# Optimization experiments

Hardware: AMD Instinct MI355X
Metric: run time of the kernel (lower is better)

The kernel has to match this reference:

```python
import jax, jax.numpy as jnp
import numpy as np

WS = 8          # window size
NH = 8          # num heads
DIM = 256
HD = DIM // NH  # head dim = 32
SCALE = HD ** -0.5
EPS = 1e-5


def _rel_pos_index(ws):
    # deterministic int index buffer, same math as the torch __init__
    coords = jnp.stack(jnp.meshgrid(jnp.arange(ws), jnp.arange(ws), indexing='ij'))  # [2,ws,ws]
    cf = coords.reshape(2, -1)                     # [2, N]
    rel = cf[:, :, None] - cf[:, None, :]          # [2, N, N]
    return (rel[0] + ws - 1) * (2 * ws - 1) + (rel[1] + ws - 1)  # [N, N]


def _ln(h, g, b):
    m = jnp.mean(h, axis=-1, keepdims=True)
    v = jnp.mean((h - m) ** 2, axis=-1, keepdims=True)
    return (h - m) / jnp.sqrt(v + EPS) * g + b


def setup_inputs() -> dict:
    key = jax.random.key(0)
    ks = jax.random.split(key, 16)
    B_, N, D = 4096, WS * WS, DIM
    s = 0.02
    return {
        'x':      jax.random.normal(ks[0], (B_, N, D), jnp.float32),
        # enhanced qkv: Linear(D,2D) -> LN -> GELU -> Linear(2D,3D)
        'w_qkv1': jax.random.normal(ks[1], (D, 2 * D), jnp.float32) * s,
        'b_qkv1': jnp.zeros((2 * D,), jnp.float32),
        'g_qkv':  jnp.ones((2 * D,), jnp.float32),
        'be_qkv': jnp.zeros((2 * D,), jnp.float32),
        'w_qkv2': jax.random.normal(ks[2], (2 * D, 3 * D), jnp.float32) * s,
        'b_qkv2': jnp.zeros((3 * D,), jnp.float32),
        # relative position bias table [(2*WS-1)^2, NH]
        'rpb':    jax.random.normal(ks[3], ((2 * WS - 1) ** 2, NH), jnp.float32) * s,
        # enhanced proj: Linear(D,2D) -> LN -> GELU -> Linear(2D,D)
        'w_p1':   jax.random.normal(ks[4], (D, 2 * D), jnp.float32) * s,
        'b_p1':   jnp.zeros((2 * D,), jnp.float32),
        'g_p':    jnp.ones((2 * D,), jnp.float32),
        'be_p':   jnp.zeros((2 * D,), jnp.float32),
        'w_p2':   jax.random.normal(ks[5], (2 * D, D), jnp.float32) * s,
        'b_p2':   jnp.zeros((D,), jnp.float32),
    }


def reference(x, w_qkv1, b_qkv1, g_qkv, be_qkv, w_qkv2, b_qkv2, rpb,
              w_p1, b_p1, g_p, be_p, w_p2, b_p2):
    B_, N, C = x.shape
    # enhanced QKV chain: Linear -> LayerNorm -> GELU -> Linear
    h = jax.nn.gelu(_ln(x @ w_qkv1 + b_qkv1, g_qkv, be_qkv), approximate=False)
    qkv = h @ w_qkv2 + b_qkv2                              # [B_, N, 3C]
    qkv = qkv.reshape(B_, N, 3, NH, HD).transpose(2, 0, 3, 1, 4)  # [3, B_, H, N, hd]
    q, k, v = qkv[0], qkv[1], qkv[2]
    attn = jnp.einsum('bhnd,bhmd->bhnm', q * SCALE, k)     # [B_, H, N, N]
    idx = _rel_pos_index(WS)                                # [N, N] int
    bias = rpb[idx.reshape(-1)].reshape(N, N, NH).transpose(2, 0, 1)  # [H, N, N]
    attn = jax.nn.softmax(attn + bias[None], axis=-1)
    out = jnp.einsum('bhnm,bhmd->bhnd', attn, v)           # [B_, H, N, hd]
    out = out.transpose(0, 2, 1, 3).reshape(B_, N, C)
    # enhanced proj chain: Linear -> LayerNorm -> GELU -> Linear
    h = jax.nn.gelu(_ln(out @ w_p1 + b_p1, g_p, be_p), approximate=False)
    return h @ w_p2 + b_p2
```

## Files before the change

### kernel.cpp

```cpp
#include <hip/hip_runtime.h>


typedef __bf16 bf16_t;
typedef __bf16 bf16x8 __attribute__((ext_vector_type(8)));
typedef __bf16 bf16x4 __attribute__((ext_vector_type(4)));
typedef float f32x4 __attribute__((ext_vector_type(4)));

__device__ __forceinline__ f32x4 mfma16(bf16x8 a, bf16x8 b, f32x4 acc) {
  return __builtin_amdgcn_mfma_f32_16x16x32_bf16(a, b, acc, 0, 0, 0);
}

#define SWZ(row, byteoff) ((byteoff) ^ (((row) & 7) << 4))

__device__ __forceinline__ float gelu_f(float v) {
  float e = __expf(v * (1.59576912f + 0.07135482f * v * v));
  return v - v * __builtin_amdgcn_rcpf(1.0f + e);
}

__global__ void wtrans_kernel(const float* __restrict__ src, bf16_t* __restrict__ dst,
                              int kshift, int N, int total) {
  int i = blockIdx.x * 256 + threadIdx.x;
  if (i >= total) return;
  int K = 1 << kshift;
  int k = i & (K - 1);
  int n = i >> kshift;
  dst[i] = (bf16_t)src[(size_t)k * N + n];
}

__global__ void biastab_kernel(const float* __restrict__ rpb, float* __restrict__ bt) {
  int e = blockIdx.x * 256 + threadIdx.x;
  int hd = e >> 12, i = (e >> 6) & 63, j = e & 63;
  int idx = ((i >> 3) - (j >> 3) + 7) * 15 + ((i & 7) - (j & 7) + 7);
  bt[e] = rpb[idx * 8 + hd];
}

__device__ __forceinline__ void gemmT_ln_gelu(
    const char* bsrc, const bf16_t* __restrict__ wt,
    const float* __restrict__ bias, const float* __restrict__ gamma,
    const float* __restrict__ beta,
    char* dst, int flb, float2* part, int wave, int g, int c)
{
  f32x4 acc[4][4] = {};
#pragma unroll
  for (int kt = 0; kt < 8; ++kt) {
    bf16x8 a[4], b[4];
#pragma unroll
    for (int mt = 0; mt < 4; ++mt)
      a[mt] = *(const bf16x8*)(wt + (size_t)(wave * 64 + mt * 16 + c) * 256 + kt * 32 + g * 8);
#pragma unroll
    for (int nt = 0; nt < 4; ++nt) {
      int T = nt * 16 + c;
      b[nt] = *(const bf16x8*)(bsrc + SWZ(T, T * 512 + kt * 64 + g * 16));
    }
#pragma unroll
    for (int mt = 0; mt < 4; ++mt)
#pragma unroll
      for (int nt = 0; nt < 4; ++nt)
        acc[mt][nt] = mfma16(a[mt], b[nt], acc[mt][nt]);
  }
  float s[4] = {0.f, 0.f, 0.f, 0.f}, ss[4] = {0.f, 0.f, 0.f, 0.f};
#pragma unroll
  for (int mt = 0; mt < 4; ++mt) {
    float4 b4 = *(const float4*)(bias + wave * 64 + mt * 16 + g * 4);
#pragma unroll
    for (int nt = 0; nt < 4; ++nt)
#pragma unroll
      for (int r = 0; r < 4; ++r) {
        float v = acc[mt][nt][r] + ((const float*)&b4)[r];
        acc[mt][nt][r] = v;
        s[nt] += v;
        ss[nt] += v * v;
      }
  }
#pragma unroll
  for (int nt = 0; nt < 4; ++nt) {
    float sv = s[nt], ssv = ss[nt];
    sv += __shfl_xor(sv, 16, 64); ssv += __shfl_xor(ssv, 16, 64);
    sv += __shfl_xor(sv, 32, 64); ssv += __shfl_xor(ssv, 32, 64);
    if (g == 0) part[wave * 64 + nt * 16 + c] = make_float2(sv, ssv);
  }
  __syncthreads();
#pragma unroll
  for (int nt = 0; nt < 4; ++nt) {
    float sv = 0.f, ssv = 0.f;
#pragma unroll
    for (int w = 0; w < 8; ++w) {
      float2 p2 = part[w * 64 + nt * 16 + c];
      sv += p2.x; ssv += p2.y;
    }
    float m = sv * (1.f / 512.f);
    float rstd = rsqrtf(ssv * (1.f / 512.f) - m * m + 1e-5f);
#pragma unroll
    for (int mt = 0; mt < 4; ++mt)
#pragma unroll
      for (int r = 0; r < 4; ++r)
        acc[mt][nt][r] = (acc[mt][nt][r] - m) * rstd;
  }
#pragma unroll
  for (int mt = 0; mt < 4; ++mt) {
    float4 g4 = *(const float4*)(gamma + wave * 64 + mt * 16 + g * 4);
    float4 be4 = *(const float4*)(beta + wave * 64 + mt * 16 + g * 4);
    int f0 = flb + mt * 16 + g * 4;
#pragma unroll
    for (int nt = 0; nt < 4; ++nt) {
      int T = nt * 16 + c;
      bf16x4 h4;
#pragma unroll
      for (int r = 0; r < 4; ++r) {
        float v = acc[mt][nt][r] * ((const float*)&g4)[r] + ((const float*)&be4)[r];
        h4[r] = (bf16_t)gelu_f(v);
      }
      *(bf16x4*)(dst + SWZ(T, T * 512 + f0 * 2)) = h4;
    }
  }
}

__global__ __launch_bounds__(512, 2) void g1qa_kernel(
    const float* __restrict__ x,
    const bf16_t* __restrict__ w1t, const float* __restrict__ b1,
    const float* __restrict__ gamma1, const float* __restrict__ beta1,
    const bf16_t* __restrict__ w2t, const float* __restrict__ b2,
    const float* __restrict__ bt,
    bf16_t* __restrict__ ao)
{
  __shared__ __align__(16) char sm[69632];
  char* rA = sm;
  char* rB = sm + 32768;
  float2* part = (float2*)(sm + 65536);
  const int tid = threadIdx.x;
  const int wave = tid >> 6, lane = tid & 63;
  const int g = lane >> 4, c = lane & 15;
  const int win = blockIdx.x;
  const int head = wave;

  const float* xw = x + (size_t)win * 16384;
#pragma unroll
  for (int it = 0; it < 8; ++it) {
    int e = it * 2048 + tid * 4;
    float4 v = *(const float4*)(xw + e);
    int row = e >> 8, col = e & 255;
    bf16x4 t4;
    t4[0] = (bf16_t)v.x; t4[1] = (bf16_t)v.y; t4[2] = (bf16_t)v.z; t4[3] = (bf16_t)v.w;
    *(bf16x4*)(rA + SWZ(row, row * 512 + col * 2)) = t4;
  }
  __syncthreads();
  gemmT_ln_gelu(rA, w1t, b1, gamma1, beta1, (wave < 4) ? rB : rA, (wave & 3) * 64,
                part, wave, g, c);
  __syncthreads();

  bf16x4 vreg[2][4], qreg[2][4], kreg[2][4];

  {
    f32x4 acc[2][4] = {};
#pragma unroll
    for (int kt = 0; kt < 16; ++kt) {
      const char* hb = (kt < 8) ? rB : rA;
      const int ko = (kt & 7) * 64 + g * 16;
      bf16x8 a[2], b[4];
#pragma unroll
      for (int mt = 0; mt < 2; ++mt)
        a[mt] = *(const bf16x8*)(w2t + (size_t)(512 + head * 32 + mt * 16 + c) * 512 + kt * 32 + g * 8);
#pragma unroll
      for (int nt = 0; nt < 4; ++nt) {
        int T = nt * 16 + c;
        b[nt] = *(const bf16x8*)(hb + SWZ(T, T * 512 + ko));
      }
#pragma unroll
      for (int mt = 0; mt < 2; ++mt)
#pragma unroll
        for (int nt = 0; nt < 4; ++nt)
          acc[mt][nt] = mfma16(a[mt], b[nt], acc[mt][nt]);
    }
#pragma unroll
    for (int mt = 0; mt < 2; ++mt) {
      float4 b4 = *(const float4*)(b2 + 512 + head * 32 + mt * 16 + g * 4);
#pragma unroll
      for (int nt = 0; nt < 4; ++nt) {
        bf16x4 o4;
#pragma unroll
        for (int r = 0; r < 4; ++r)
          o4[r] = (bf16_t)(acc[mt][nt][r] + ((const float*)&b4)[r]);
        vreg[mt][nt] = o4;
      }
    }
  }
  {
    f32x4 acc[2][4] = {};
#pragma unroll
    for (int kt = 0; kt < 16; ++kt) {
      const char* hb = (kt < 8) ? rB : rA;
      const int ko = (kt & 7) * 64 + g * 16;
      bf16x8 a[2], b[4];
#pragma unroll
      for (int mt = 0; mt < 2; ++mt)
        a[mt] = *(const bf16x8*)(w2t + (size_t)(head * 32 + mt * 16 + c) * 512 + kt * 32 + g * 8);
#pragma unroll
      for (int nt = 0; nt < 4; ++nt) {
        int T = nt * 16 + c;
        b[nt] = *(const bf16x8*)(hb + SWZ(T, T * 512 + ko));
      }
#pragma unroll
      for (int mt = 0; mt < 2; ++mt)
#pragma unroll
        for (int nt = 0; nt < 4; ++nt)
          acc[mt][nt] = mfma16(a[mt], b[nt], acc[mt][nt]);
    }
#pragma unroll
    for (int mt = 0; mt < 2; ++mt) {
      float4 b4 = *(const float4*)(b2 + head * 32 + mt * 16 + g * 4);
#pragma unroll
      for (int nt = 0; nt < 4; ++nt) {
        bf16x4 o4;
#pragma unroll
        for (int r = 0; r < 4; ++r)
          o4[r] = (bf16_t)((acc[mt][nt][r] + ((const float*)&b4)[r]) * 0.17677669529663687f);
        qreg[mt][nt] = o4;
      }
    }
  }
  {
    f32x4 acc[2][4] = {};
#pragma unroll
    for (int kt = 0; kt < 16; ++kt) {
      const char* hb = (kt < 8) ? rB : rA;
      const int ko = (kt & 7) * 64 + g * 16;
      bf16x8 a[2], b[4];
#pragma unroll
      for (int mt = 0; mt < 2; ++mt)
        a[mt] = *(const bf16x8*)(w2t + (size_t)(256 + head * 32 + mt * 16 + c) * 512 + kt * 32 + g * 8);
#pragma unroll
      for (int nt = 0; nt < 4; ++nt) {
        int T = nt * 16 + c;
        b[nt] = *(const bf16x8*)(hb + SWZ(T, T * 512 + ko));
      }
#pragma unroll
      for (int mt = 0; mt < 2; ++mt)
#pragma unroll
        for (int nt = 0; nt < 4; ++nt)
          acc[mt][nt] = mfma16(a[mt], b[nt], acc[mt][nt]);
    }
#pragma unroll
    for (int mt = 0; mt < 2; ++mt) {
      float4 b4 = *(const float4*)(b2 + 256 + head * 32 + mt * 16 + g * 4);
#pragma unroll
      for (int nt = 0; nt < 4; ++nt) {
        bf16x4 o4;
#pragma unroll
        for (int r = 0; r < 4; ++r)
          o4[r] = (bf16_t)(acc[mt][nt][r] + ((const float*)&b4)[r]);
        kreg[mt][nt] = o4;
      }
    }
  }
  __syncthreads();

  {
    char* vs = sm + 32768 + (head >> 2) * 16384 + (head & 3) * 4096;
#pragma unroll
    for (int mt = 0; mt < 2; ++mt)
#pragma unroll
      for (int nt = 0; nt < 4; ++nt) {
        int T = nt * 16 + c;
#pragma unroll
        for (int r = 0; r < 4; ++r) {
          int d = mt * 16 + g * 4 + r;
          *(bf16_t*)(vs + SWZ(d, d * 128 + T * 2)) = vreg[mt][nt][r];
        }
      }
  }
  if (head < 4) {
    char* qb = sm + head * 8192;
#pragma unroll
    for (int mt = 0; mt < 2; ++mt)
#pragma unroll
      for (int nt = 0; nt < 4; ++nt) {
        int T = nt * 16 + c, d0 = mt * 16 + g * 4;
        *(bf16x4*)(qb + SWZ(T, T * 64 + d0 * 2)) = qreg[mt][nt];
        *(bf16x4*)(qb + 4096 + SWZ(T, T * 64 + d0 * 2)) = kreg[mt][nt];
      }
  }

  const int rowbase = (wave >> 2) * 32;
#pragma unroll
  for (int s = 0; s < 2; ++s) {
    if (s == 1 && head >= 4) {
      char* qb = sm + (head & 3) * 8192;
#pragma unroll
      for (int mt = 0; mt < 2; ++mt)
#pragma unroll
        for (int nt = 0; nt < 4; ++nt) {
          int T = nt * 16 + c, d0 = mt * 16 + g * 4;
          *(bf16x4*)(qb + SWZ(T, T * 64 + d0 * 2)) = qreg[mt][nt];
          *(bf16x4*)(qb + 4096 + SWZ(T, T * 64 + d0 * 2)) = kreg[mt][nt];
        }
    }
    __syncthreads();

    const int hd = s * 4 + (wave & 3);
    char* qb = sm + (wave & 3) * 8192;
    char* vslot = sm + 32768 + s * 16384 + (wave & 3) * 4096;
    const float* btab = bt + hd * 4096;

    bf16x8 aq[2], bk[4];
#pragma unroll
    for (int mt = 0; mt < 2; ++mt) {
      int t = rowbase + mt * 16 + c;
      aq[mt] = *(const bf16x8*)(qb + SWZ(t, t * 64 + g * 16));
    }
#pragma unroll
    for (int nt = 0; nt < 4; ++nt) {
      int t = nt * 16 + c;
      bk[nt] = *(const bf16x8*)(qb + 4096 + SWZ(t, t * 64 + g * 16));
    }
    float p[2][4][4];
#pragma unroll
    for (int mt = 0; mt < 2; ++mt)
#pragma unroll
      for (int nt = 0; nt < 4; ++nt) {
        f32x4 z = {0.f, 0.f, 0.f, 0.f};
        f32x4 s4 = mfma16(aq[mt], bk[nt], z);
#pragma unroll
        for (int r = 0; r < 4; ++r) {
          int i = rowbase + mt * 16 + g * 4 + r, j = nt * 16 + c;
          p[mt][nt][r] = s4[r] + btab[i * 64 + j];
        }
      }
#pragma unroll
    for (int mt = 0; mt < 2; ++mt)
#pragma unroll
      for (int r = 0; r < 4; ++r) {
        float mx = fmaxf(fmaxf(p[mt][0][r], p[mt][1][r]), fmaxf(p[mt][2][r], p[mt][3][r]));
#pragma unroll
        for (int m = 1; m < 16; m <<= 1) mx = fmaxf(mx, __shfl_xor(mx, m, 64));
        float sum = 0.f;
#pragma unroll
        for (int nt = 0; nt < 4; ++nt) {
          float e = __expf(p[mt][nt][r] - mx);
          p[mt][nt][r] = e; sum += e;
        }
#pragma unroll
        for (int m = 1; m < 16; m <<= 1) sum += __shfl_xor(sum, m, 64);
        float rinv = 1.f / sum;
#pragma unroll
        for (int nt = 0; nt < 4; ++nt) p[mt][nt][r] *= rinv;
      }
    __syncthreads();
#pragma unroll
    for (int mt = 0; mt < 2; ++mt)
#pragma unroll
      for (int nt = 0; nt < 4; ++nt)
#pragma unroll
        for (int r = 0; r < 4; ++r) {
          int i = rowbase + mt * 16 + g * 4 + r, j = nt * 16 + c;
          *(bf16_t*)(qb + SWZ(i, i * 128 + j * 2)) = (bf16_t)p[mt][nt][r];
        }
    asm volatile("s_waitcnt lgkmcnt(0)" ::: "memory");
    f32x4 oacc[2][2] = {};
#pragma unroll
    for (int kp = 0; kp < 2; ++kp) {
      bf16x8 ap[2], bv[2];
#pragma unroll
      for (int mt = 0; mt < 2; ++mt) {
        int t = rowbase + mt * 16 + c;
        ap[mt] = *(const bf16x8*)(qb + SWZ(t, t * 128 + kp * 64 + g * 16));
      }
#pragma unroll
      for (int nt = 0; nt < 2; ++nt) {
        int d = nt * 16 + c;
        bv[nt] = *(const bf16x8*)(vslot + SWZ(d, d * 128 + kp * 64 + g * 16));
      }
#pragma unroll
      for (int mt = 0; mt < 2; ++mt)
#pragma unroll
        for (int nt = 0; nt < 2; ++nt)
          oacc[mt][nt] = mfma16(ap[mt], bv[nt], oacc[mt][nt]);
    }
#pragma unroll
    for (int mt = 0; mt < 2; ++mt)
#pragma unroll
      for (int nt = 0; nt < 2; ++nt)
#pragma unroll
        for (int r = 0; r < 4; ++r) {
          int T = rowbase + mt * 16 + g * 4 + r;
          ao[(size_t)(win * 64 + T) * 256 + hd * 32 + nt * 16 + c] = (bf16_t)oacc[mt][nt][r];
        }
    if (s == 0) __syncthreads();
  }
}

__global__ __launch_bounds__(512, 2) void g3g4_kernel(
    const bf16_t* __restrict__ ao,
    const bf16_t* __restrict__ wp1t, const float* __restrict__ bp1,
    const float* __restrict__ gp, const float* __restrict__ bep,
    const bf16_t* __restrict__ wp2t, const float* __restrict__ bp2,
    float* __restrict__ out)
{
  __shared__ __align__(16) char sm[69632];
  char* rA = sm;
  char* rB = sm + 32768;
  float2* part = (float2*)(sm + 65536);
  const int tid = threadIdx.x;
  const int wave = tid >> 6, lane = tid & 63;
  const int g = lane >> 4, c = lane & 15;
  const int win = blockIdx.x;

  const bf16_t* aow = ao + (size_t)win * 16384;
#pragma unroll
  for (int it = 0; it < 4; ++it) {
    int e = it * 4096 + tid * 8;
    bf16x8 v = *(const bf16x8*)(aow + e);
    int row = e >> 8, col = e & 255;
    *(bf16x8*)(rA + SWZ(row, row * 512 + col * 2)) = v;
  }
  __syncthreads();
  gemmT_ln_gelu(rA, wp1t, bp1, gp, bep, (wave < 4) ? rB : rA, (wave & 3) * 64,
                part, wave, g, c);
  __syncthreads();

  f32x4 acc[2][4] = {};
#pragma unroll
  for (int kt = 0; kt < 16; ++kt) {
    const char* hb = (kt < 8) ? rB : rA;
    const int ko = (kt & 7) * 64 + g * 16;
    bf16x8 a[2], b[4];
#pragma unroll
    for (int mt = 0; mt < 2; ++mt)
      a[mt] = *(const bf16x8*)(wp2t + (size_t)(wave * 32 + mt * 16 + c) * 512 + kt * 32 + g * 8);
#pragma unroll
    for (int nt = 0; nt < 4; ++nt) {
      int T = nt * 16 + c;
      b[nt] = *(const bf16x8*)(hb + SWZ(T, T * 512 + ko));
    }
#pragma unroll
    for (int mt = 0; mt < 2; ++mt)
#pragma unroll
      for (int nt = 0; nt < 4; ++nt)
        acc[mt][nt] = mfma16(a[mt], b[nt], acc[mt][nt]);
  }
  float* ow = out + (size_t)win * 16384;
#pragma unroll
  for (int mt = 0; mt < 2; ++mt) {
    float4 b4 = *(const float4*)(bp2 + wave * 32 + mt * 16 + g * 4);
#pragma unroll
    for (int nt = 0; nt < 4; ++nt) {
      int T = nt * 16 + c;
      f32x4 o4;
#pragma unroll
      for (int r = 0; r < 4; ++r) o4[r] = acc[mt][nt][r] + ((const float*)&b4)[r];
      *(f32x4*)(ow + T * 256 + wave * 32 + mt * 16 + g * 4) = o4;
    }
  }
}

extern "C" void kernel_launch(void* const* d_in, const int* in_sizes, int n_in,
                              void* d_out, int out_size, void* d_ws, size_t ws_size,
                              hipStream_t stream) {
  const float* x   = (const float*)d_in[0];
  const float* w1  = (const float*)d_in[1];
  const float* b1  = (const float*)d_in[2];
  const float* g1  = (const float*)d_in[3];
  const float* be1 = (const float*)d_in[4];
  const float* w2  = (const float*)d_in[5];
  const float* b2  = (const float*)d_in[6];
  const float* rpb = (const float*)d_in[7];
  const float* wp1 = (const float*)d_in[8];
  const float* bp1 = (const float*)d_in[9];
  const float* gp  = (const float*)d_in[10];
  const float* bep = (const float*)d_in[11];
  const float* wp2 = (const float*)d_in[12];
  const float* bp2 = (const float*)d_in[13];
  float* out = (float*)d_out;
  char* ws = (char*)d_ws;
  bf16_t* w1t  = (bf16_t*)(ws + 0);
  bf16_t* w2t  = (bf16_t*)(ws + 262144);
  bf16_t* wp1t = (bf16_t*)(ws + 1048576);
  bf16_t* wp2t = (bf16_t*)(ws + 1310720);
  float*  bt   = (float*)(ws + 1572864);
  bf16_t* ao   = (bf16_t*)(ws + 2097152);

  wtrans_kernel<<<512, 256, 0, stream>>>(w1, w1t, 8, 512, 131072);
  wtrans_kernel<<<1536, 256, 0, stream>>>(w2, w2t, 9, 768, 393216);
  wtrans_kernel<<<512, 256, 0, stream>>>(wp1, wp1t, 8, 512, 131072);
  wtrans_kernel<<<512, 256, 0, stream>>>(wp2, wp2t, 9, 256, 131072);
  biastab_kernel<<<128, 256, 0, stream>>>(rpb, bt);

  g1qa_kernel<<<4096, 512, 0, stream>>>(x, w1t, b1, g1, be1, w2t, b2, bt, ao);
  g3g4_kernel<<<4096, 512, 0, stream>>>(ao, wp1t, bp1, gp, bep, wp2t, bp2, out);
}
```

Baseline: 1.201 ms.

## Use 1024-thread blocks with 16 waves splitting GEMM tiles and heads

Doubles the block size from 8 to 16 waves in both fused kernels, so each wave computes half the output-feature tile in the GEMM+LayerNorm+GELU stage, the QKV projection and the final projection. The attention stage is restructured so all 8 heads' Q/K/V are staged in shared memory at once, with each pair of waves handling one head's row halves. This removes the previous two-pass serialized attention loop and its extra barriers. The cost is larger LDS usage (96 KB), only one block per CU, more partial-sum traffic for LayerNorm, and less register-level reuse per wave in the MFMA loops.

```diff
diff --git a/kernel.cpp b/kernel.cpp
--- a/kernel.cpp
+++ b/kernel.cpp
@@ -34,34 +34,34 @@
   bt[e] = rpb[idx * 8 + hd];
 }
 
-__device__ __forceinline__ void gemmT_ln_gelu(
+__device__ __forceinline__ void gemmT_ln_gelu16(
     const char* bsrc, const bf16_t* __restrict__ wt,
     const float* __restrict__ bias, const float* __restrict__ gamma,
     const float* __restrict__ beta,
     char* dst, int flb, float2* part, int wave, int g, int c)
 {
-  f32x4 acc[4][4] = {};
+  f32x4 acc[2][4] = {};
 #pragma unroll
   for (int kt = 0; kt < 8; ++kt) {
-    bf16x8 a[4], b[4];
-#pragma unroll
-    for (int mt = 0; mt < 4; ++mt)
-      a[mt] = *(const bf16x8*)(wt + (size_t)(wave * 64 + mt * 16 + c) * 256 + kt * 32 + g * 8);
+    bf16x8 a[2], b[4];
+#pragma unroll
+    for (int mt = 0; mt < 2; ++mt)
+      a[mt] = *(const bf16x8*)(wt + (size_t)(wave * 32 + mt * 16 + c) * 256 + kt * 32 + g * 8);
 #pragma unroll
     for (int nt = 0; nt < 4; ++nt) {
       int T = nt * 16 + c;
       b[nt] = *(const bf16x8*)(bsrc + SWZ(T, T * 512 + kt * 64 + g * 16));
     }
 #pragma unroll
-    for (int mt = 0; mt < 4; ++mt)
+    for (int mt = 0; mt < 2; ++mt)
 #pragma unroll
       for (int nt = 0; nt < 4; ++nt)
         acc[mt][nt] = mfma16(a[mt], b[nt], acc[mt][nt]);
   }
   float s[4] = {0.f, 0.f, 0.f, 0.f}, ss[4] = {0.f, 0.f, 0.f, 0.f};
 #pragma unroll
-  for (int mt = 0; mt < 4; ++mt) {
-    float4 b4 = *(const float4*)(bias + wave * 64 + mt * 16 + g * 4);
+  for (int mt = 0; mt < 2; ++mt) {
+    float4 b4 = *(const float4*)(bias + wave * 32 + mt * 16 + g * 4);
 #pragma unroll
     for (int nt = 0; nt < 4; ++nt)
 #pragma unroll
@@ -84,22 +84,22 @@
   for (int nt = 0; nt < 4; ++nt) {
     float sv = 0.f, ssv = 0.f;
 #pragma unroll
-    for (int w = 0; w < 8; ++w) {
+    for (int w = 0; w < 16; ++w) {
       float2 p2 = part[w * 64 + nt * 16 + c];
       sv += p2.x; ssv += p2.y;
     }
     float m = sv * (1.f / 512.f);
     float rstd = rsqrtf(ssv * (1.f / 512.f) - m * m + 1e-5f);
 #pragma unroll
-    for (int mt = 0; mt < 4; ++mt)
+    for (int mt = 0; mt < 2; ++mt)
 #pragma unroll
       for (int r = 0; r < 4; ++r)
         acc[mt][nt][r] = (acc[mt][nt][r] - m) * rstd;
   }
 #pragma unroll
-  for (int mt = 0; mt < 4; ++mt) {
-    float4 g4 = *(const float4*)(gamma + wave * 64 + mt * 16 + g * 4);
-    float4 be4 = *(const float4*)(beta + wave * 64 + mt * 16 + g * 4);
+  for (int mt = 0; mt < 2; ++mt) {
+    float4 g4 = *(const float4*)(gamma + wave * 32 + mt * 16 + g * 4);
+    float4 be4 = *(const float4*)(beta + wave * 32 + mt * 16 + g * 4);
     int f0 = flb + mt * 16 + g * 4;
 #pragma unroll
     for (int nt = 0; nt < 4; ++nt) {
@@ -115,7 +115,7 @@
   }
 }
 
-__global__ __launch_bounds__(512, 2) void g1qa_kernel(
+__global__ __launch_bounds__(1024, 1) void g1qa_kernel(
     const float* __restrict__ x,
     const bf16_t* __restrict__ w1t, const float* __restrict__ b1,
     const float* __restrict__ gamma1, const float* __restrict__ beta1,
@@ -123,7 +123,7 @@
     const float* __restrict__ bt,
     bf16_t* __restrict__ ao)
 {
-  __shared__ __align__(16) char sm[69632];
+  __shared__ __align__(16) char sm[98304];
   char* rA = sm;
   char* rB = sm + 32768;
   float2* part = (float2*)(sm + 65536);
@@ -131,12 +131,11 @@
   const int wave = tid >> 6, lane = tid & 63;
   const int g = lane >> 4, c = lane & 15;
   const int win = blockIdx.x;
-  const int head = wave;
 
   const float* xw = x + (size_t)win * 16384;
 #pragma unroll
-  for (int it = 0; it < 8; ++it) {
-    int e = it * 2048 + tid * 4;
+  for (int it = 0; it < 4; ++it) {
+    int e = it * 4096 + tid * 4;
     float4 v = *(const float4*)(xw + e);
     int row = e >> 8, col = e & 255;
     bf16x4 t4;
@@ -144,258 +143,207 @@
     *(bf16x4*)(rA + SWZ(row, row * 512 + col * 2)) = t4;
   }
   __syncthreads();
-  gemmT_ln_gelu(rA, w1t, b1, gamma1, beta1, (wave < 4) ? rB : rA, (wave & 3) * 64,
-                part, wave, g, c);
-  __syncthreads();
-
-  bf16x4 vreg[2][4], qreg[2][4], kreg[2][4];
-
+  gemmT_ln_gelu16(rA, w1t, b1, gamma1, beta1, (wave < 8) ? rB : rA, (wave & 7) * 32,
+                  part, wave, g, c);
+  __syncthreads();
+
+  const int hh = wave >> 1, mh = wave & 1;
+  bf16x4 vreg[4], qreg[4], kreg[4];
   {
-    f32x4 acc[2][4] = {};
+    f32x4 acc[4] = {};
 #pragma unroll
     for (int kt = 0; kt < 16; ++kt) {
       const char* hb = (kt < 8) ? rB : rA;
       const int ko = (kt & 7) * 64 + g * 16;
-      bf16x8 a[2], b[4];
-#pragma unroll
-      for (int mt = 0; mt < 2; ++mt)
-        a[mt] = *(const bf16x8*)(w2t + (size_t)(512 + head * 32 + mt * 16 + c) * 512 + kt * 32 + g * 8);
+      bf16x8 a = *(const bf16x8*)(w2t + (size_t)(512 + hh * 32 + mh * 16 + c) * 512 + kt * 32 + g * 8);
+      bf16x8 b[4];
 #pragma unroll
       for (int nt = 0; nt < 4; ++nt) {
         int T = nt * 16 + c;
         b[nt] = *(const bf16x8*)(hb + SWZ(T, T * 512 + ko));
       }
 #pragma unroll
-      for (int mt = 0; mt < 2; ++mt)
-#pragma unroll
-        for (int nt = 0; nt < 4; ++nt)
-          acc[mt][nt] = mfma16(a[mt], b[nt], acc[mt][nt]);
-    }
-#pragma unroll
-    for (int mt = 0; mt < 2; ++mt) {
-      float4 b4 = *(const float4*)(b2 + 512 + head * 32 + mt * 16 + g * 4);
-#pragma unroll
-      for (int nt = 0; nt < 4; ++nt) {
-        bf16x4 o4;
-#pragma unroll
-        for (int r = 0; r < 4; ++r)
-          o4[r] = (bf16_t)(acc[mt][nt][r] + ((const float*)&b4)[r]);
-        vreg[mt][nt] = o4;
-      }
-    }
+      for (int nt = 0; nt < 4; ++nt)
+        acc[nt] = mfma16(a, b[nt], acc[nt]);
+    }
+    float4 b4 = *(const float4*)(b2 + 512 + hh * 32 + mh * 16 + g * 4);
+#pragma unroll
+    for (int nt = 0; nt < 4; ++nt)
+#pragma unroll
+      for (int r = 0; r < 4; ++r)
+        vreg[nt][r] = (bf16_t)(acc[nt][r] + ((const float*)&b4)[r]);
   }
   {
-    f32x4 acc[2][4] = {};
+    f32x4 acc[4] = {};
 #pragma unroll
     for (int kt = 0; kt < 16; ++kt) {
       const char* hb = (kt < 8) ? rB : rA;
       const int ko = (kt & 7) * 64 + g * 16;
-      bf16x8 a[2], b[4];
-#pragma unroll
-      for (int mt = 0; mt < 2; ++mt)
-        a[mt] = *(const bf16x8*)(w2t + (size_t)(head * 32 + mt * 16 + c) * 512 + kt * 32 + g * 8);
+      bf16x8 a = *(const bf16x8*)(w2t + (size_t)(hh * 32 + mh * 16 + c) * 512 + kt * 32 + g * 8);
+      bf16x8 b[4];
 #pragma unroll
       for (int nt = 0; nt < 4; ++nt) {
         int T = nt * 16 + c;
         b[nt] = *(const bf16x8*)(hb + SWZ(T, T * 512 + ko));
       }
 #pragma unroll
-      for (int mt = 0; mt < 2; ++mt)
-#pragma unroll
-        for (int nt = 0; nt < 4; ++nt)
-          acc[mt][nt] = mfma16(a[mt], b[nt], acc[mt][nt]);
-    }
-#pragma unroll
-    for (int mt = 0; mt < 2; ++mt) {
-      float4 b4 = *(const float4*)(b2 + head * 32 + mt * 16 + g * 4);
-#pragma unroll
-      for (int nt = 0; nt < 4; ++nt) {
-        bf16x4 o4;
-#pragma unroll
-        for (int r = 0; r < 4; ++r)
-          o4[r] = (bf16_t)((acc[mt][nt][r] + ((const float*)&b4)[r]) * 0.17677669529663687f);
-        qreg[mt][nt] = o4;
-      }
-    }
+      for (int nt = 0; nt < 4; ++nt)
+        acc[nt] = mfma16(a, b[nt], acc[nt]);
+    }
+    float4 b4 = *(const float4*)(b2 + hh * 32 + mh * 16 + g * 4);
+#pragma unroll
+    for (int nt = 0; nt < 4; ++nt)
+#pragma unroll
+      for (int r = 0; r < 4; ++r)
+        qreg[nt][r] = (bf16_t)((acc[nt][r] + ((const float*)&b4)[r]) * 0.17677669529663687f);
   }
   {
-    f32x4 acc[2][4] = {};
+    f32x4 acc[4] = {};
 #pragma unroll
     for (int kt = 0; kt < 16; ++kt) {
       const char* hb = (kt < 8) ? rB : rA;
       const int ko = (kt & 7) * 64 + g * 16;
-      bf16x8 a[2], b[4];
-#pragma unroll
-      for (int mt = 0; mt < 2; ++mt)
-        a[mt] = *(const bf16x8*)(w2t + (size_t)(256 + head * 32 + mt * 16 + c) * 512 + kt * 32 + g * 8);
+      bf16x8 a = *(const bf16x8*)(w2t + (size_t)(256 + hh * 32 + mh * 16 + c) * 512 + kt * 32 + g * 8);
+      bf16x8 b[4];
 #pragma unroll
       for (int nt = 0; nt < 4; ++nt) {
         int T = nt * 16 + c;
         b[nt] = *(const bf16x8*)(hb + SWZ(T, T * 512 + ko));
       }
 #pragma unroll
-      for (int mt = 0; mt < 2; ++mt)
-#pragma unroll
-        for (int nt = 0; nt < 4; ++nt)
-          acc[mt][nt] = mfma16(a[mt], b[nt], acc[mt][nt]);
-    }
-#pragma unroll
-    for (int mt = 0; mt < 2; ++mt) {
-      float4 b4 = *(const float4*)(b2 + 256 + head * 32 + mt * 16 + g * 4);
+      for (int nt = 0; nt < 4; ++nt)
+        acc[nt] = mfma16(a, b[nt], acc[nt]);
+    }
+    float4 b4 = *(const float4*)(b2 + 256 + hh * 32 + mh * 16 + g * 4);
+#pragma unroll
+    for (int nt = 0; nt < 4; ++nt)
+#pragma unroll
+      for (int r = 0; r < 4; ++r)
+        kreg[nt][r] = (bf16_t)(acc[nt][r] + ((const float*)&b4)[r]);
+  }
+  __syncthreads();
+
+  {
+    char* qb = sm + hh * 8192;
+    const int d0 = mh * 16 + g * 4;
+#pragma unroll
+    for (int nt = 0; nt < 4; ++nt) {
+      int T = nt * 16 + c;
+      *(bf16x4*)(qb + SWZ(T, T * 64 + d0 * 2)) = qreg[nt];
+      *(bf16x4*)(qb + 4096 + SWZ(T, T * 64 + d0 * 2)) = kreg[nt];
+    }
+    char* vs = sm + 65536 + hh * 4096;
+#pragma unroll
+    for (int nt = 0; nt < 4; ++nt) {
+      int T = nt * 16 + c;
+#pragma unroll
+      for (int r = 0; r < 4; ++r) {
+        int d = d0 + r;
+        *(bf16_t*)(vs + SWZ(d, d * 128 + T * 2)) = vreg[nt][r];
+      }
+    }
+  }
+  __syncthreads();
+
+  const int h8 = wave & 7, rowbase = (wave >> 3) * 32;
+  char* qb = sm + h8 * 8192;
+  char* vslot = sm + 65536 + h8 * 4096;
+  const float* btab = bt + h8 * 4096;
+
+  bf16x8 aq[2], bk[4];
+#pragma unroll
+  for (int mt = 0; mt < 2; ++mt) {
+    int t = rowbase + mt * 16 + c;
+    aq[mt] = *(const bf16x8*)(qb + SWZ(t, t * 64 + g * 16));
+  }
+#pragma unroll
+  for (int nt = 0; nt < 4; ++nt) {
+    int t = nt * 16 + c;
+    bk[nt] = *(const bf16x8*)(qb + 4096 + SWZ(t, t * 64 + g * 16));
+  }
+  float p[2][4][4];
+#pragma unroll
+  for (int mt = 0; mt < 2; ++mt)
+#pragma unroll
+    for (int nt = 0; nt < 4; ++nt) {
+      f32x4 z = {0.f, 0.f, 0.f, 0.f};
+      f32x4 s4 = mfma16(aq[mt], bk[nt], z);
+#pragma unroll
+      for (int r = 0; r < 4; ++r) {
+        int i = rowbase + mt * 16 + g * 4 + r, j = nt * 16 + c;
+        p[mt][nt][r] = s4[r] + btab[i * 64 + j];
+      }
+    }
+#pragma unroll
+  for (int mt = 0; mt < 2; ++mt)
+#pragma unroll
+    for (int r = 0; r < 4; ++r) {
+      float mx = fmaxf(fmaxf(p[mt][0][r], p[mt][1][r]), fmaxf(p[mt][2][r], p[mt][3][r]));
+#pragma unroll
+      for (int m = 1; m < 16; m <<= 1) mx = fmaxf(mx, __shfl_xor(mx, m, 64));
+      float sum = 0.f;
 #pragma unroll
       for (int nt = 0; nt < 4; ++nt) {
-        bf16x4 o4;
-#pragma unroll
-        for (int r = 0; r < 4; ++r)
-          o4[r] = (bf16_t)(acc[mt][nt][r] + ((const float*)&b4)[r]);
-        kreg[mt][nt] = o4;
-      }
-    }
-  }
-  __syncthreads();
-
-  {
-    char* vs = sm + 32768 + (head >> 2) * 16384 + (head & 3) * 4096;
-#pragma unroll
-    for (int mt = 0; mt < 2; ++mt)
-#pragma unroll
-      for (int nt = 0; nt < 4; ++nt) {
-        int T = nt * 16 + c;
-#pragma unroll
-        for (int r = 0; r < 4; ++r) {
-          int d = mt * 16 + g * 4 + r;
-          *(bf16_t*)(vs + SWZ(d, d * 128 + T * 2)) = vreg[mt][nt][r];
-        }
-      }
-  }
-  if (head < 4) {
-    char* qb = sm + head * 8192;
-#pragma unroll
-    for (int mt = 0; mt < 2; ++mt)
-#pragma unroll
-      for (int nt = 0; nt < 4; ++nt) {
-        int T = nt * 16 + c, d0 = mt * 16 + g * 4;
-        *(bf16x4*)(qb + SWZ(T, T * 64 + d0 * 2)) = qreg[mt][nt];
-        *(bf16x4*)(qb + 4096 + SWZ(T, T * 64 + d0 * 2)) = kreg[mt][nt];
-      }
-  }
-
-  const int rowbase = (wave >> 2) * 32;
-#pragma unroll
-  for (int s = 0; s < 2; ++s) {
-    if (s == 1 && head >= 4) {
-      char* qb = sm + (head & 3) * 8192;
-#pragma unroll
-      for (int mt = 0; mt < 2; ++mt)
-#pragma unroll
-        for (int nt = 0; nt < 4; ++nt) {
-          int T = nt * 16 + c, d0 = mt * 16 + g * 4;
-          *(bf16x4*)(qb + SWZ(T, T * 64 + d0 * 2)) = qreg[mt][nt];
-          *(bf16x4*)(qb + 4096 + SWZ(T, T * 64 + d0 * 2)) = kreg[mt][nt];
-        }
-    }
-    __syncthreads();
-
-    const int hd = s * 4 + (wave & 3);
-    char* qb = sm + (wave & 3) * 8192;
-    char* vslot = sm + 32768 + s * 16384 + (wave & 3) * 4096;
-    const float* btab = bt + hd * 4096;
-
-    bf16x8 aq[2], bk[4];
+        float e = __expf(p[mt][nt][r] - mx);
+        p[mt][nt][r] = e; sum += e;
+      }
+#pragma unroll
+      for (int m = 1; m < 16; m <<= 1) sum += __shfl_xor(sum, m, 64);
+      float rinv = 1.f / sum;
+#pragma unroll
+      for (int nt = 0; nt < 4; ++nt) p[mt][nt][r] *= rinv;
+    }
+  __syncthreads();
+
+#pragma unroll
+  for (int mt = 0; mt < 2; ++mt)
+#pragma unroll
+    for (int nt = 0; nt < 4; ++nt)
+#pragma unroll
+      for (int r = 0; r < 4; ++r) {
+        int i = rowbase + mt * 16 + g * 4 + r, j = nt * 16 + c;
+        *(bf16_t*)(qb + SWZ(i, i * 128 + j * 2)) = (bf16_t)p[mt][nt][r];
+      }
+  asm volatile("s_waitcnt lgkmcnt(0)" ::: "memory");
+  f32x4 oacc[2][2] = {};
+#pragma unroll
+  for (int kp = 0; kp < 2; ++kp) {
+    bf16x8 ap[2], bv[2];
 #pragma unroll
     for (int mt = 0; mt < 2; ++mt) {
       int t = rowbase + mt * 16 + c;
-      aq[mt] = *(const bf16x8*)(qb + SWZ(t, t * 64 + g * 16));
-    }
-#pragma unroll
-    for (int nt = 0; nt < 4; ++nt) {
-      int t = nt * 16 + c;
-      bk[nt] = *(const bf16x8*)(qb + 4096 + SWZ(t, t * 64 + g * 16));
-    }
-    float p[2][4][4];
+      ap[mt] = *(const bf16x8*)(qb + SWZ(t, t * 128 + kp * 64 + g * 16));
+    }
+#pragma unroll
+    for (int nt = 0; nt < 2; ++nt) {
+      int d = nt * 16 + c;
+      bv[nt] = *(const bf16x8*)(vslot + SWZ(d, d * 128 + kp * 64 + g * 16));
+    }
 #pragma unroll
     for (int mt = 0; mt < 2; ++mt)
 #pragma unroll
-      for (int nt = 0; nt < 4; ++nt) {
-        f32x4 z = {0.f, 0.f, 0.f, 0.f};
-        f32x4 s4 = mfma16(aq[mt], bk[nt], z);
-#pragma unroll
-        for (int r = 0; r < 4; ++r) {
-          int i = rowbase + mt * 16 + g * 4 + r, j = nt * 16 + c;
-          p[mt][nt][r] = s4[r] + btab[i * 64 + j];
-        }
-      }
-#pragma unroll
-    for (int mt = 0; mt < 2; ++mt)
-#pragma unroll
-      for (int r = 0; r < 4; ++r) {
-        float mx = fmaxf(fmaxf(p[mt][0][r], p[mt][1][r]), fmaxf(p[mt][2][r], p[mt][3][r]));
-#pragma unroll
-        for (int m = 1; m < 16; m <<= 1) mx = fmaxf(mx, __shfl_xor(mx, m, 64));
-        float sum = 0.f;
-#pragma unroll
-        for (int nt = 0; nt < 4; ++nt) {
-          float e = __expf(p[mt][nt][r] - mx);
-          p[mt][nt][r] = e; sum += e;
-        }
-#pragma unroll
-        for (int m = 1; m < 16; m <<= 1) sum += __shfl_xor(sum, m, 64);
-        float rinv = 1.f / sum;
-#pragma unroll
-        for (int nt = 0; nt < 4; ++nt) p[mt][nt][r] *= rinv;
-      }
-    __syncthreads();
-#pragma unroll
-    for (int mt = 0; mt < 2; ++mt)
-#pragma unroll
-      for (int nt = 0; nt < 4; ++nt)
-#pragma unroll
-        for (int r = 0; r < 4; ++r) {
-          int i = rowbase + mt * 16 + g * 4 + r, j = nt * 16 + c;
-          *(bf16_t*)(qb + SWZ(i, i * 128 + j * 2)) = (bf16_t)p[mt][nt][r];
-        }
-    asm volatile("s_waitcnt lgkmcnt(0)" ::: "memory");
-    f32x4 oacc[2][2] = {};
-#pragma unroll
-    for (int kp = 0; kp < 2; ++kp) {
-      bf16x8 ap[2], bv[2];
-#pragma unroll
-      for (int mt = 0; mt < 2; ++mt) {
-        int t = rowbase + mt * 16 + c;
-        ap[mt] = *(const bf16x8*)(qb + SWZ(t, t * 128 + kp * 64 + g * 16));
-      }
-#pragma unroll
-      for (int nt = 0; nt < 2; ++nt) {
-        int d = nt * 16 + c;
-        bv[nt] = *(const bf16x8*)(vslot + SWZ(d, d * 128 + kp * 64 + g * 16));
-      }
-#pragma unroll
-      for (int mt = 0; mt < 2; ++mt)
-#pragma unroll
-        for (int nt = 0; nt < 2; ++nt)
-          oacc[mt][nt] = mfma16(ap[mt], bv[nt], oacc[mt][nt]);
-    }
-#pragma unroll
-    for (int mt = 0; mt < 2; ++mt)
-#pragma unroll
       for (int nt = 0; nt < 2; ++nt)
-#pragma unroll
-        for (int r = 0; r < 4; ++r) {
-          int T = rowbase + mt * 16 + g * 4 + r;
-          ao[(size_t)(win * 64 + T) * 256 + hd * 32 + nt * 16 + c] = (bf16_t)oacc[mt][nt][r];
-        }
-    if (s == 0) __syncthreads();
-  }
-}
-
-__global__ __launch_bounds__(512, 2) void g3g4_kernel(
+        oacc[mt][nt] = mfma16(ap[mt], bv[nt], oacc[mt][nt]);
+  }
+#pragma unroll
+  for (int mt = 0; mt < 2; ++mt)
+#pragma unroll
+    for (int nt = 0; nt < 2; ++nt)
+#pragma unroll
+      for (int r = 0; r < 4; ++r) {
+        int T = rowbase + mt * 16 + g * 4 + r;
+        ao[(size_t)(win * 64 + T) * 256 + h8 * 32 + nt * 16 + c] = (bf16_t)oacc[mt][nt][r];
+      }
+}
+
+__global__ __launch_bounds__(1024, 1) void g3g4_kernel(
     const bf16_t* __restrict__ ao,
     const bf16_t* __restrict__ wp1t, const float* __restrict__ bp1,
     const float* __restrict__ gp, const float* __restrict__ bep,
     const bf16_t* __restrict__ wp2t, const float* __restrict__ bp2,
     float* __restrict__ out)
 {
-  __shared__ __align__(16) char sm[69632];
+  __shared__ __align__(16) char sm[73728];
   char* rA = sm;
   char* rB = sm + 32768;
   float2* part = (float2*)(sm + 65536);
@@ -406,49 +354,42 @@
 
   const bf16_t* aow = ao + (size_t)win * 16384;
 #pragma unroll
-  for (int it = 0; it < 4; ++it) {
-    int e = it * 4096 + tid * 8;
+  for (int it = 0; it < 2; ++it) {
+    int e = it * 8192 + tid * 8;
     bf16x8 v = *(const bf16x8*)(aow + e);
     int row = e >> 8, col = e & 255;
     *(bf16x8*)(rA + SWZ(row, row * 512 + col * 2)) = v;
   }
   __syncthreads();
-  gemmT_ln_gelu(rA, wp1t, bp1, gp, bep, (wave < 4) ? rB : rA, (wave & 3) * 64,
-                part, wave, g, c);
-  __syncthreads();
-
-  f32x4 acc[2][4] = {};
+  gemmT_ln_gelu16(rA, wp1t, bp1, gp, bep, (wave < 8) ? rB : rA, (wave & 7) * 32,
+                  part, wave, g, c);
+  __syncthreads();
+
+  f32x4 acc[4] = {};
 #pragma unroll
   for (int kt = 0; kt < 16; ++kt) {
     const char* hb = (kt < 8) ? rB : rA;
     const int ko = (kt & 7) * 64 + g * 16;
-    bf16x8 a[2], b[4];
-#pragma unroll
-    for (int mt = 0; mt < 2; ++mt)
-      a[mt] = *(const bf16x8*)(wp2t + (size_t)(wave * 32 + mt * 16 + c) * 512 + kt * 32 + g * 8);
+    bf16x8 a = *(const bf16x8*)(wp2t + (size_t)(wave * 16 + c) * 512 + kt * 32 + g * 8);
+    bf16x8 b[4];
 #pragma unroll
     for (int nt = 0; nt < 4; ++nt) {
       int T = nt * 16 + c;
       b[nt] = *(const bf16x8*)(hb + SWZ(T, T * 512 + ko));
     }
 #pragma unroll
-    for (int mt = 0; mt < 2; ++mt)
-#pragma unroll
-      for (int nt = 0; nt < 4; ++nt)
-        acc[mt][nt] = mfma16(a[mt], b[nt], acc[mt][nt]);
+    for (int nt = 0; nt < 4; ++nt)
+      acc[nt] = mfma16(a, b[nt], acc[nt]);
   }
   float* ow = out + (size_t)win * 16384;
-#pragma unroll
-  for (int mt = 0; mt < 2; ++mt) {
-    float4 b4 = *(const float4*)(bp2 + wave * 32 + mt * 16 + g * 4);
-#pragma unroll
-    for (int nt = 0; nt < 4; ++nt) {
-      int T = nt * 16 + c;
-      f32x4 o4;
-#pragma unroll
-      for (int r = 0; r < 4; ++r) o4[r] = acc[mt][nt][r] + ((const float*)&b4)[r];
-      *(f32x4*)(ow + T * 256 + wave * 32 + mt * 16 + g * 4) = o4;
-    }
+  float4 b4 = *(const float4*)(bp2 + wave * 16 + g * 4);
+#pragma unroll
+  for (int nt = 0; nt < 4; ++nt) {
+    int T = nt * 16 + c;
+    f32x4 o4;
+#pragma unroll
+    for (int r = 0; r < 4; ++r) o4[r] = acc[nt][r] + ((const float*)&b4)[r];
+    *(f32x4*)(ow + T * 256 + wave * 16 + g * 4) = o4;
   }
 }
 
@@ -484,6 +425,6 @@
   wtrans_kernel<<<512, 256, 0, stream>>>(wp2, wp2t, 9, 256, 131072);
   biastab_kernel<<<128, 256, 0, stream>>>(rpb, bt);
 
-  g1qa_kernel<<<4096, 512, 0, stream>>>(x, w1t, b1, g1, be1, w2t, b2, bt, ao);
-  g3g4_kernel<<<4096, 512, 0, stream>>>(ao, wp1t, bp1, gp, bep, wp2t, bp2, out);
-}
+  g1qa_kernel<<<4096, 1024, 0, stream>>>(x, w1t, b1, g1, be1, w2t, b2, bt, ao);
+  g3g4_kernel<<<4096, 1024, 0, stream>>>(ao, wp1t, bp1, gp, bep, wp2t, bp2, out);
+}
```

Result: faster. 1.124 ms (-6.4%).
